# Kernel optimization log

Hardware: AMD Instinct MI355X
Metric: run time of the kernel (lower is better)

The kernel has to match this reference:

```python
import jax, jax.numpy as jnp
import numpy as np

EMBED_DIM = 1024
NUM_HEADS = 16
HEAD_DIM = EMBED_DIM // NUM_HEADS


def setup_inputs() -> dict:
    key = jax.random.key(0)
    ks = jax.random.split(key, 11)
    B, S, D = 2, 2048, EMBED_DIM
    s = 1.0 / np.sqrt(D)
    inp = {
        "query": jax.random.normal(ks[0], (B, S, D), jnp.float32),
        "key": jax.random.normal(ks[1], (B, S, D), jnp.float32),
        "value": jax.random.normal(ks[2], (B, S, D), jnp.float32),
        # torch Linear weights: [out, in]
        "Wq": jax.random.normal(ks[3], (D, D), jnp.float32) * s,
        "bq": jnp.zeros((D,), jnp.float32),
        "Wk": jax.random.normal(ks[4], (D, D), jnp.float32) * s,
        "bk": jnp.zeros((D,), jnp.float32),
        "Wv": jax.random.normal(ks[5], (D, D), jnp.float32) * s,
        "bv": jnp.zeros((D,), jnp.float32),
        "Wo": jax.random.normal(ks[6], (D, D), jnp.float32) * s,
        "bo": jnp.zeros((D,), jnp.float32),
    }
    return inp


def reference(query, key, value, Wq, bq, Wk, bk, Wv, bv, Wo, bo):
    B, Q, D = query.shape
    K = key.shape[1]
    H, Hd = NUM_HEADS, HEAD_DIM
    # NOTE: source divides by scaling = head_dim**-0.5, i.e. multiplies by sqrt(head_dim)
    scaling = float(Hd) ** (-0.5)

    q = (query @ Wq.T + bq).reshape(B, Q, H, Hd).transpose(0, 2, 1, 3)  # [B,H,Q,Hd]
    k = (key @ Wk.T + bk).reshape(B, K, H, Hd).transpose(0, 2, 1, 3)    # [B,H,K,Hd]
    v = (value @ Wv.T + bv).reshape(B, K, H, Hd).transpose(0, 2, 1, 3)  # [B,H,K,Hd]

    scores = jnp.einsum("bhqd,bhkd->bhqk", q, k) / scaling
    attn = jax.nn.softmax(scores, axis=-1)  # dropout=0 (eval)
    out = jnp.einsum("bhqk,bhkd->bhqd", attn, v)
    out = out.transpose(0, 2, 1, 3).reshape(B, Q, D)
    return out @ Wo.T + bo
```

## Files before the change

### kernel.cpp

```cpp
#include <hip/hip_runtime.h>
#include <type_traits>
#include <utility>

#define B_ 2
#define S_ 2048
#define D_ 1024
#define H_ 16
#define HD_ 64
#define KDIM 1024

typedef __attribute__((ext_vector_type(8))) short    s16x8;
typedef __attribute__((ext_vector_type(8))) _Float16 h16x8;
typedef __attribute__((ext_vector_type(4))) float    f32x4;
typedef __attribute__((ext_vector_type(16))) float   f32x16;
typedef __attribute__((ext_vector_type(4))) int      i32x4;
typedef __attribute__((ext_vector_type(2))) int      i32x2;

template <typename T, typename = void> struct mfma_takes : std::false_type {};
template <typename T>
struct mfma_takes<T, std::void_t<decltype(__builtin_amdgcn_mfma_f32_16x16x32_f16(
    std::declval<T>(), std::declval<T>(), std::declval<f32x4>(), 0, 0, 0))>>
    : std::true_type {};
using frag8 = std::conditional_t<mfma_takes<h16x8>::value, h16x8, s16x8>;

__device__ __forceinline__ f32x4 mfma_f16(frag8 a, frag8 b, f32x4 c) {
  return __builtin_amdgcn_mfma_f32_16x16x32_f16(a, b, c, 0, 0, 0);
}
__device__ __forceinline__ f32x16 mfma32(frag8 a, frag8 b, f32x16 c) {
  return __builtin_amdgcn_mfma_f32_32x32x16_f16(a, b, c, 0, 0, 0);
}

__device__ __forceinline__ short f2h(float f) {
  _Float16 h = (_Float16)f;
  short s; __builtin_memcpy(&s, &h, 2);
  return s;
}
__device__ __forceinline__ int pk2h(float a, float b) {
  auto p = __builtin_amdgcn_cvt_pkrtz(a, b);
  int r; __builtin_memcpy(&r, &p, 4); return r;
}
__device__ __forceinline__ frag8 ld_frag(const short* p) {
  return __builtin_bit_cast(frag8, *(const i32x4*)p);
}
__device__ __forceinline__ float fast_exp2(float x) {
  return __builtin_amdgcn_exp2f(x);
}
__device__ __forceinline__ void pl32swap(int& a, int& b) {
  asm volatile("v_permlane32_swap_b32 %0, %1" : "+v"(a), "+v"(b));
}

typedef __attribute__((address_space(1))) const void gvoid;
typedef __attribute__((address_space(3))) void lvoid;
__device__ __forceinline__ void async_copy16(const void* g, void* l) {
  __builtin_amdgcn_global_load_lds((gvoid*)g, (lvoid*)l, 16, 0, 0);
}

#define RAW_BARRIER() asm volatile("s_barrier" ::: "memory")
#define WAITCNT_VM(n) asm volatile("s_waitcnt vmcnt(" #n ")" ::: "memory")

__global__ __launch_bounds__(256)
void conv_w(const float* __restrict__ Wq, const float* __restrict__ Wk,
            const float* __restrict__ Wv, const float* __restrict__ Wo,
            short* __restrict__ wq, short* __restrict__ wk,
            short* __restrict__ wv, short* __restrict__ wo) {
  const int blk = blockIdx.x;
  const float* src; short* dst; int base;
  if (blk < 512)        { src = Wq; dst = wq; base = blk; }
  else if (blk < 1024)  { src = Wk; dst = wk; base = blk - 512; }
  else if (blk < 1536)  { src = Wv; dst = wv; base = blk - 1024; }
  else                  { src = Wo; dst = wo; base = blk - 1536; }
  const int i = base * 2048 + threadIdx.x * 8;
  float4 a0 = *(const float4*)(src + i);
  float4 a1 = *(const float4*)(src + i + 4);
  short h[8] = { f2h(a0.x), f2h(a0.y), f2h(a0.z), f2h(a0.w),
                 f2h(a1.x), f2h(a1.y), f2h(a1.z), f2h(a1.w) };
  i32x4 ph; __builtin_memcpy(&ph, h, 16);
  *(i32x4*)(dst + i) = ph;
}

__global__ __launch_bounds__(256, 3)
void gemm_qkv(const float* __restrict__ Aq, const float* __restrict__ Ak,
              const float* __restrict__ Av, const short* __restrict__ wq,
              const short* __restrict__ wk, const short* __restrict__ wv,
              const float* __restrict__ bq, const float* __restrict__ bk,
              const float* __restrict__ bv, short* __restrict__ Qf,
              short* __restrict__ Kf, short* __restrict__ Vt, float QS) {
  __shared__ short As[3 * 4096];
  __shared__ short Bs[3 * 4096];

  const int blk = blockIdx.x;
  const int xcd = blk & 7, i = blk >> 3;
  const int p = (i >> 3) * 8 + xcd;
  const int bn = i & 7;
  const int z = p >> 5, bm = p & 31;
  const float* Af = z == 0 ? Aq : z == 1 ? Ak : Av;
  const short* Wp = z == 0 ? wq : z == 1 ? wk : wv;
  const float* bias = z == 0 ? bq : z == 1 ? bk : bv;
  short* Out = z == 0 ? Qf : z == 1 ? Kf : Vt;
  const float scale = z == 0 ? QS : 1.0f;
  const int omode = z == 2 ? 2 : 1;

  const int t = threadIdx.x, wave = t >> 6, lane = t & 63;
  const int laneN = lane & 15, quad = lane >> 4;
  const int wm = wave & 1, wn = wave >> 1;

  f32x4 acc[4][4];
#pragma unroll
  for (int i2 = 0; i2 < 4; ++i2)
#pragma unroll
    for (int j = 0; j < 4; ++j)
#pragma unroll
      for (int r = 0; r < 4; ++r) acc[i2][j][r] = 0.f;

  const int ch0 = t, ch1 = 256 + t;
  const int ar0 = ch0 >> 2, ag0 = (ch0 & 3) ^ ((ar0 >> 1) & 3);
  const int ar1 = ch1 >> 2, ag1 = (ch1 & 3) ^ ((ar1 >> 1) & 3);
  const float* ap0 = Af + (size_t)(bm * 128 + ar0) * KDIM + ag0 * 8;
  const float* ap1 = Af + (size_t)(bm * 128 + ar1) * KDIM + ag1 * 8;

  f32x4 rA0a, rA0b, rA1a, rA1b;

  auto loadA = [&](int kk) {
    rA0a = *(const f32x4*)(ap0 + kk);
    rA0b = *(const f32x4*)(ap0 + kk + 4);
    rA1a = *(const f32x4*)(ap1 + kk);
    rA1b = *(const f32x4*)(ap1 + kk + 4);
  };
  auto writeA = [&](int slot) {
    short pk[8];
    pk[0] = f2h(rA0a[0]); pk[1] = f2h(rA0a[1]);
    pk[2] = f2h(rA0a[2]); pk[3] = f2h(rA0a[3]);
    pk[4] = f2h(rA0b[0]); pk[5] = f2h(rA0b[1]);
    pk[6] = f2h(rA0b[2]); pk[7] = f2h(rA0b[3]);
    i32x4 w0; __builtin_memcpy(&w0, pk, 16);
    *(i32x4*)(As + slot * 4096 + ch0 * 8) = w0;
    pk[0] = f2h(rA1a[0]); pk[1] = f2h(rA1a[1]);
    pk[2] = f2h(rA1a[2]); pk[3] = f2h(rA1a[3]);
    pk[4] = f2h(rA1b[0]); pk[5] = f2h(rA1b[1]);
    pk[6] = f2h(rA1b[2]); pk[7] = f2h(rA1b[3]);
    i32x4 w1; __builtin_memcpy(&w1, pk, 16);
    *(i32x4*)(As + slot * 4096 + ch1 * 8) = w1;
  };
  auto stageB = [&](int slot, int kk) {
#pragma unroll
    for (int j = 0; j < 2; ++j) {
      const int chunk = j * 256 + t;
      const int row = chunk >> 2;
      const int gg = (chunk & 3) ^ ((row >> 1) & 3);
      async_copy16(Wp + (size_t)(bn * 128 + row) * KDIM + kk + gg * 8,
                   Bs + slot * 4096 + chunk * 8);
    }
  };

  loadA(0);
  writeA(0);
  loadA(32);
  stageB(0, 0);
  stageB(1, 32);

  int buf = 0;
  for (int kk = 0; kk < KDIM; kk += 32) {
    if (kk + 64 < KDIM) {
      WAITCNT_VM(2);
      int ns = buf + 1; if (ns >= 3) ns -= 3;
      writeA(ns);
      loadA(kk + 64);
      int nb = buf + 2; if (nb >= 3) nb -= 3;
      stageB(nb, kk + 64);
    } else if (kk + 32 < KDIM) {
      WAITCNT_VM(2);
      int ns = buf + 1; if (ns >= 3) ns -= 3;
      writeA(ns);
    } else {
      WAITCNT_VM(0);
    }
    RAW_BARRIER();

    frag8 aF[4], bF[4];
#pragma unroll
    for (int mi = 0; mi < 4; ++mi) {
      const int row = wm * 64 + mi * 16 + laneN;
      aF[mi] = ld_frag(As + buf * 4096 + row * 32 +
                       ((quad ^ ((row >> 1) & 3)) * 8));
    }
#pragma unroll
    for (int ni = 0; ni < 4; ++ni) {
      const int row = wn * 64 + ni * 16 + laneN;
      bF[ni] = ld_frag(Bs + buf * 4096 + row * 32 +
                       ((quad ^ ((row >> 1) & 3)) * 8));
    }
#pragma unroll
    for (int mi = 0; mi < 4; ++mi)
#pragma unroll
      for (int ni = 0; ni < 4; ++ni)
        acc[mi][ni] = mfma_f16(aF[mi], bF[ni], acc[mi][ni]);
    RAW_BARRIER();
    buf = buf + 1 == 3 ? 0 : buf + 1;
  }

  short* scr = As + wave * 1152;
  const int h = bn * 2 + wn;
  if (omode == 2) {
    const int bidx = bm >> 4;
    const int sbase = (bm * 128 + wm * 64) & 2047;
#pragma unroll
    for (int ni = 0; ni < 4; ++ni) {
      const float bb = bias[bn * 128 + wn * 64 + ni * 16 + laneN];
#pragma unroll
      for (int mi = 0; mi < 4; ++mi) {
        short pk[4];
#pragma unroll
        for (int r = 0; r < 4; ++r) pk[r] = f2h(acc[mi][ni][r] + bb);
        i32x2 w; __builtin_memcpy(&w, pk, 8);
        *(i32x2*)(scr + laneN * 72 + mi * 16 + quad * 4) = w;
      }
#pragma unroll
      for (int j = 0; j < 2; ++j) {
        const int ff = lane * 2 + j, hdr = ff >> 3, ch = ff & 7;
        i32x4 v = *(const i32x4*)(scr + hdr * 72 + ch * 8);
        *(i32x4*)(Vt + (((size_t)(bidx * H_ + h)) * HD_ + ni * 16 + hdr) * S_ +
                  sbase + ch * 8) = v;
      }
    }
  } else {
#pragma unroll
    for (int mi = 0; mi < 4; ++mi) {
#pragma unroll
      for (int ni = 0; ni < 4; ++ni) {
        const float bb = bias[bn * 128 + wn * 64 + ni * 16 + laneN];
#pragma unroll
        for (int r = 0; r < 4; ++r)
          scr[(quad * 4 + r) * 72 + ni * 16 + laneN] =
              f2h((acc[mi][ni][r] + bb) * scale);
      }
#pragma unroll
      for (int j = 0; j < 2; ++j) {
        const int ff = lane * 2 + j, row = ff >> 3, ch = ff & 7;
        const int rowg = bm * 128 + wm * 64 + mi * 16 + row;
        const int bidx = rowg >> 11, s = rowg & 2047;
        i32x4 v = *(const i32x4*)(scr + row * 72 + ch * 8);
        *(i32x4*)(Out + (((size_t)(bidx * H_ + h)) * S_ + s) * HD_ + ch * 8) = v;
      }
    }
  }
}

__global__ __launch_bounds__(256, 3)
void gemm_out(const short* __restrict__ Ap, const short* __restrict__ Wp,
              const float* __restrict__ bias, float* __restrict__ Out) {
  __shared__ short As[2 * 8192];
  __shared__ short Bs[2 * 4096];
  const int blk = blockIdx.x;
  const int xcd = blk & 7, i = blk >> 3;
  const int bm = (i >> 4) * 8 + xcd;
  const int bn = i & 15;

  const int t = threadIdx.x, wave = t >> 6, lane = t & 63;
  const int laneN = lane & 15, quad = lane >> 4;
  const int wm = wave & 1, wn = wave >> 1;

  f32x4 acc[4][2];
#pragma unroll
  for (int i2 = 0; i2 < 4; ++i2)
#pragma unroll
    for (int j = 0; j < 2; ++j)
#pragma unroll
      for (int r = 0; r < 4; ++r) acc[i2][j][r] = 0.f;

  auto stage = [&](int buf, int kk) {
#pragma unroll
    for (int j = 0; j < 4; ++j) {
      const int c = j * 256 + t;
      const int row = c >> 3, g = (c & 7) ^ (row & 7);
      async_copy16(Ap + (size_t)(bm * 128 + row) * KDIM + kk + g * 8,
                   As + buf * 8192 + c * 8);
    }
#pragma unroll
    for (int j = 0; j < 2; ++j) {
      const int c = j * 256 + t;
      const int row = c >> 3, g = (c & 7) ^ (row & 7);
      async_copy16(Wp + (size_t)(bn * 64 + row) * KDIM + kk + g * 8,
                   Bs + buf * 4096 + c * 8);
    }
  };

  int offA[4][2], offB[2][2];
#pragma unroll
  for (int mi = 0; mi < 4; ++mi) {
    const int row = wm * 64 + mi * 16 + laneN;
#pragma unroll
    for (int ks = 0; ks < 2; ++ks)
      offA[mi][ks] = row * 64 + (((quad + 4 * ks) ^ (row & 7)) * 8);
  }
#pragma unroll
  for (int ni = 0; ni < 2; ++ni) {
    const int row = wn * 32 + ni * 16 + laneN;
#pragma unroll
    for (int ks = 0; ks < 2; ++ks)
      offB[ni][ks] = row * 64 + (((quad + 4 * ks) ^ (row & 7)) * 8);
  }

  stage(0, 0);
  int buf = 0;
  for (int kk = 0; kk < KDIM; kk += 64) {
    if (kk + 64 < KDIM) {
      stage(buf ^ 1, kk + 64);
      WAITCNT_VM(6);
    } else {
      WAITCNT_VM(0);
    }
    RAW_BARRIER();

    frag8 aF[4][2], bF[2][2];
#pragma unroll
    for (int mi = 0; mi < 4; ++mi) {
      aF[mi][0] = ld_frag(As + buf * 8192 + offA[mi][0]);
      aF[mi][1] = ld_frag(As + buf * 8192 + offA[mi][1]);
    }
#pragma unroll
    for (int ni = 0; ni < 2; ++ni) {
      bF[ni][0] = ld_frag(Bs + buf * 4096 + offB[ni][0]);
      bF[ni][1] = ld_frag(Bs + buf * 4096 + offB[ni][1]);
    }
#pragma unroll
    for (int mi = 0; mi < 4; ++mi)
#pragma unroll
      for (int ni = 0; ni < 2; ++ni) {
        acc[mi][ni] = mfma_f16(aF[mi][0], bF[ni][0], acc[mi][ni]);
        acc[mi][ni] = mfma_f16(aF[mi][1], bF[ni][1], acc[mi][ni]);
      }
    RAW_BARRIER();
    buf ^= 1;
  }

  float* scr = (float*)As + wave * 576;
#pragma unroll
  for (int mi = 0; mi < 4; ++mi) {
#pragma unroll
    for (int ni = 0; ni < 2; ++ni) {
      const float bb = bias[bn * 64 + wn * 32 + ni * 16 + laneN];
#pragma unroll
      for (int r = 0; r < 4; ++r)
        scr[(quad * 4 + r) * 36 + ni * 16 + laneN] = acc[mi][ni][r] + bb;
    }
#pragma unroll
    for (int j = 0; j < 2; ++j) {
      const int ff = lane * 2 + j, row = ff >> 3, ch = ff & 7;
      const int rowg = bm * 128 + wm * 64 + mi * 16 + row;
      f32x4 v = *(const f32x4*)(scr + row * 36 + ch * 4);
      *(f32x4*)(Out + (size_t)rowg * 1024 + bn * 64 + wn * 32 + ch * 4) = v;
    }
  }
}

__global__ __launch_bounds__(256, 2)
void attn(const short* __restrict__ Qf, const short* __restrict__ Kf,
          const short* __restrict__ Vt_, short* __restrict__ Ow) {
  __shared__ short Ks[4 * 4096];
  __shared__ short Vts[4 * 4096];

  const int blk = blockIdx.x;
  const int xcd = blk & 7, local = blk >> 3;
  const int pair = xcd * 4 + (local >> 4);
  const int h = pair & 15, b = pair >> 4, qt = local & 15;
  const size_t head = ((size_t)b * H_ + h) * (size_t)S_ * HD_;

  const int t = threadIdx.x;
  const int wave = t >> 6, lane = t & 63;
  const int l31 = lane & 31, hi = lane >> 5;

  const int q0 = qt * 128 + wave * 32;

  frag8 qf[4];
  {
    const short* qp = Qf + head + (size_t)(q0 + l31) * HD_ + hi * 8;
#pragma unroll
    for (int ds = 0; ds < 4; ++ds) qf[ds] = ld_frag(qp + ds * 16);
  }

  f32x16 o0, o1;
#pragma unroll
  for (int r = 0; r < 16; ++r) { o0[r] = 0.f; o1[r] = 0.f; }
  float m_r = -1e30f, l_r = 0.f;

  const int c0 = t, c1 = 256 + t;
  const int r0 = c0 >> 3, gg0 = (c0 & 7) ^ (r0 & 7);
  const int r1 = c1 >> 3, gg1 = (c1 & 7) ^ (r1 & 7);
  const short* kp0 = Kf + head + (size_t)r0 * HD_ + gg0 * 8;
  const short* kp1 = Kf + head + (size_t)r1 * HD_ + gg1 * 8;
  const short* vp0 = Vt_ + head + (size_t)r0 * S_ + gg0 * 8;
  const short* vp1 = Vt_ + head + (size_t)r1 * S_ + gg1 * 8;
  const int d0 = c0 * 8, d1 = c1 * 8;

  int off2[2][4];
#pragma unroll
  for (int hf = 0; hf < 2; ++hf) {
    const int row = hf * 32 + l31;
#pragma unroll
    for (int j = 0; j < 4; ++j)
      off2[hf][j] = row * 64 + (((j * 2 + hi) ^ (row & 7)) * 8);
  }

  async_copy16(kp0, Ks + d0);  async_copy16(kp1, Ks + d1);
  async_copy16(vp0, Vts + d0); async_copy16(vp1, Vts + d1);
  kp0 += 4096; kp1 += 4096; vp0 += 64; vp1 += 64;
  async_copy16(kp0, Ks + 4096 + d0);  async_copy16(kp1, Ks + 4096 + d1);
  async_copy16(vp0, Vts + 4096 + d0); async_copy16(vp1, Vts + 4096 + d1);
  kp0 += 4096; kp1 += 4096; vp0 += 64; vp1 += 64;

#define ATTN_TILE(B0, STG)                                                   \
  {                                                                          \
    if (STG == 1) {                                                          \
      const int nb = ((B0) + 2) & 3;                                         \
      async_copy16(kp0, Ks + nb * 4096 + d0);                                \
      async_copy16(kp1, Ks + nb * 4096 + d1);                                \
      async_copy16(vp0, Vts + nb * 4096 + d0);                               \
      async_copy16(vp1, Vts + nb * 4096 + d1);                               \
      kp0 += 4096; kp1 += 4096; vp0 += 64; vp1 += 64;                        \
      WAITCNT_VM(8);                                                         \
    } else if (STG == 2) {                                                   \
      WAITCNT_VM(4);                                                         \
    } else {                                                                 \
      WAITCNT_VM(0);                                                         \
    }                                                                        \
    RAW_BARRIER();                                                           \
    const short* KbS = Ks + (B0) * 4096;                                     \
    const short* VbS = Vts + (B0) * 4096;                                    \
                  \
    f32x16 sA, sB;                                                           \
    _Pragma("unroll")                                                        \
    for (int r = 0; r < 16; ++r) { sA[r] = 0.f; sB[r] = 0.f; }               \
    __builtin_amdgcn_s_setprio(1);                                           \
    _Pragma("unroll")                                                        \
    for (int ds = 0; ds < 4; ++ds) {                                         \
      frag8 ka = ld_frag(KbS + off2[0][ds]);                                 \
      frag8 kb = ld_frag(KbS + off2[1][ds]);                                 \
      sA = mfma32(ka, qf[ds], sA);                                           \
      sB = mfma32(kb, qf[ds], sB);                                           \
    }                                                                        \
    __builtin_amdgcn_s_setprio(0);                                           \
                 \
    {                                                                        \
      float mA = sA[0], mB = sB[0];                                          \
      _Pragma("unroll")                                                      \
      for (int r = 1; r < 16; ++r) {                                         \
        mA = fmaxf(mA, sA[r]); mB = fmaxf(mB, sB[r]);                        \
      }                                                                      \
      float mx = fmaxf(mA, mB);                                              \
      mx = fmaxf(mx, __shfl_xor(mx, 32));                                    \
      if (__any(mx > m_r + 8.f)) {                                           \
        const float mn = fmaxf(m_r, mx);                                     \
        const float al = fast_exp2(m_r - mn);                                \
        m_r = mn; l_r *= al;                                                 \
        _Pragma("unroll")                                                    \
        for (int r = 0; r < 16; ++r) { o0[r] *= al; o1[r] *= al; }           \
      }                                                                      \
      float rs = 0.f;                                                        \
      _Pragma("unroll")                                                      \
      for (int r = 0; r < 16; ++r) {                                         \
        const float pa = fast_exp2(sA[r] - m_r);                             \
        const float pb = fast_exp2(sB[r] - m_r);                             \
        sA[r] = pa; sB[r] = pb; rs += pa + pb;                               \
      }                                                                      \
      rs += __shfl_xor(rs, 32);                                              \
      l_r += rs;                                                             \
    }                                                                        \
       \
    frag8 pf0, pf1, pf2, pf3;                                                \
    {                                                                        \
      int w0, w1, w2, w3; i32x4 fw;                                          \
      w0 = pk2h(sA[0], sA[1]);   w1 = pk2h(sA[2], sA[3]);                    \
      w2 = pk2h(sA[4], sA[5]);   w3 = pk2h(sA[6], sA[7]);                    \
      pl32swap(w0, w2); pl32swap(w1, w3);                                    \
      fw[0] = w0; fw[1] = w1; fw[2] = w2; fw[3] = w3;                        \
      pf0 = __builtin_bit_cast(frag8, fw);                                   \
      w0 = pk2h(sA[8], sA[9]);   w1 = pk2h(sA[10], sA[11]);                  \
      w2 = pk2h(sA[12], sA[13]); w3 = pk2h(sA[14], sA[15]);                  \
      pl32swap(w0, w2); pl32swap(w1, w3);                                    \
      fw[0] = w0; fw[1] = w1; fw[2] = w2; fw[3] = w3;                        \
      pf1 = __builtin_bit_cast(frag8, fw);                                   \
      w0 = pk2h(sB[0], sB[1]);   w1 = pk2h(sB[2], sB[3]);                    \
      w2 = pk2h(sB[4], sB[5]);   w3 = pk2h(sB[6], sB[7]);                    \
      pl32swap(w0, w2); pl32swap(w1, w3);                                    \
      fw[0] = w0; fw[1] = w1; fw[2] = w2; fw[3] = w3;                        \
      pf2 = __builtin_bit_cast(frag8, fw);                                   \
      w0 = pk2h(sB[8], sB[9]);   w1 = pk2h(sB[10], sB[11]);                  \
      w2 = pk2h(sB[12], sB[13]); w3 = pk2h(sB[14], sB[15]);                  \
      pl32swap(w0, w2); pl32swap(w1, w3);                                    \
      fw[0] = w0; fw[1] = w1; fw[2] = w2; fw[3] = w3;                        \
      pf3 = __builtin_bit_cast(frag8, fw);                                   \
    }                                                                        \
                        \
    __builtin_amdgcn_s_setprio(1);                                           \
    {                                                                        \
      frag8 va, vb;                                                          \
      va = ld_frag(VbS + off2[0][0]); o0 = mfma32(va, pf0, o0);              \
      vb = ld_frag(VbS + off2[1][0]); o1 = mfma32(vb, pf0, o1);              \
      va = ld_frag(VbS + off2[0][1]); o0 = mfma32(va, pf1, o0);              \
      vb = ld_frag(VbS + off2[1][1]); o1 = mfma32(vb, pf1, o1);              \
      va = ld_frag(VbS + off2[0][2]); o0 = mfma32(va, pf2, o0);              \
      vb = ld_frag(VbS + off2[1][2]); o1 = mfma32(vb, pf2, o1);              \
      va = ld_frag(VbS + off2[0][3]); o0 = mfma32(va, pf3, o0);              \
      vb = ld_frag(VbS + off2[1][3]); o1 = mfma32(vb, pf3, o1);              \
    }                                                                        \
    __builtin_amdgcn_s_setprio(0);                                           \
  }

  for (int it = 0; it < 7; ++it) {
    ATTN_TILE(0, 1)
    ATTN_TILE(1, 1)
    ATTN_TILE(2, 1)
    ATTN_TILE(3, 1)
  }
  ATTN_TILE(0, 1)
  ATTN_TILE(1, 1)
  ATTN_TILE(2, 2)
  ATTN_TILE(3, 0)
#undef ATTN_TILE

  {
    const float inv = 1.0f / l_r;
    short* dst = Ow + ((size_t)b * S_ + q0 + l31) * D_ + h * HD_ + hi * 4;
#pragma unroll
    for (int rg = 0; rg < 4; ++rg) {
      i32x2 w;
      w[0] = pk2h(o0[rg * 4 + 0] * inv, o0[rg * 4 + 1] * inv);
      w[1] = pk2h(o0[rg * 4 + 2] * inv, o0[rg * 4 + 3] * inv);
      *(i32x2*)(dst + rg * 8) = w;
      i32x2 w2;
      w2[0] = pk2h(o1[rg * 4 + 0] * inv, o1[rg * 4 + 1] * inv);
      w2[1] = pk2h(o1[rg * 4 + 2] * inv, o1[rg * 4 + 3] * inv);
      *(i32x2*)(dst + 32 + rg * 8) = w2;
    }
  }
}

extern "C" void kernel_launch(void* const* d_in, const int* in_sizes, int n_in,
                              void* d_out, int out_size, void* d_ws, size_t ws_size,
                              hipStream_t stream) {
  const float* q  = (const float*)d_in[0];
  const float* k  = (const float*)d_in[1];
  const float* v  = (const float*)d_in[2];
  const float* Wq = (const float*)d_in[3];
  const float* bq = (const float*)d_in[4];
  const float* Wk = (const float*)d_in[5];
  const float* bk = (const float*)d_in[6];
  const float* Wv = (const float*)d_in[7];
  const float* bv = (const float*)d_in[8];
  const float* Wo = (const float*)d_in[9];
  const float* bo = (const float*)d_in[10];

  const size_t NTOK = (size_t)B_ * S_ * D_;
  const size_t NW   = (size_t)D_ * D_;
  short* p = (short*)d_ws;
  short* wq = p; p += NW;    short* wk = p; p += NW;
  short* wv = p; p += NW;    short* wo = p; p += NW;
  short* Qf = p; p += NTOK;  short* Kf = p; p += NTOK;
  short* Vt = p; p += NTOK;  short* Ow = p; p += NTOK;

  dim3 blk(256);

  conv_w<<<2048, blk, 0, stream>>>(Wq, Wk, Wv, Wo, wq, wk, wv, wo);

  const float QS = 11.541560327111707f;
  gemm_qkv<<<768, blk, 0, stream>>>(q, k, v, wq, wk, wv, bq, bk, bv,
                                    Qf, Kf, Vt, QS);

  attn<<<512, dim3(256), 0, stream>>>(Qf, Kf, Vt, Ow);

  gemm_out<<<512, blk, 0, stream>>>(Ow, wo, bo, (float*)d_out);
}
```

Before: 233.9 us.

## Deepen A-operand register prefetch to two stages in QKV projection GEMM

The fp32 A-tile global loads in the QKV projection GEMM are now double-buffered in registers, so each load is issued two k-steps ahead instead of one. The main loop is unrolled by two with explicit register sets, plus a peeled prologue and epilogue with adjusted vmcnt waits. This aims to hide more global-load latency behind the MFMA work. The cost is more VGPRs for the extra register stage, which could lower occupancy.

```diff
diff --git a/kernel.cpp b/kernel.cpp
--- a/kernel.cpp
+++ b/kernel.cpp
@@ -47,6 +47,12 @@
 }
 __device__ __forceinline__ void pl32swap(int& a, int& b) {
   asm volatile("v_permlane32_swap_b32 %0, %1" : "+v"(a), "+v"(b));
+}
+__device__ __forceinline__ void cvt_store8(f32x4 va, f32x4 vb, short* dst) {
+  short pk[8] = { f2h(va[0]), f2h(va[1]), f2h(va[2]), f2h(va[3]),
+                  f2h(vb[0]), f2h(vb[1]), f2h(vb[2]), f2h(vb[3]) };
+  i32x4 w; __builtin_memcpy(&w, pk, 16);
+  *(i32x4*)dst = w;
 }
 
 typedef __attribute__((address_space(1))) const void gvoid;
@@ -118,29 +124,36 @@
   const float* ap0 = Af + (size_t)(bm * 128 + ar0) * KDIM + ag0 * 8;
   const float* ap1 = Af + (size_t)(bm * 128 + ar1) * KDIM + ag1 * 8;
 
-  f32x4 rA0a, rA0b, rA1a, rA1b;
-
-  auto loadA = [&](int kk) {
-    rA0a = *(const f32x4*)(ap0 + kk);
-    rA0b = *(const f32x4*)(ap0 + kk + 4);
-    rA1a = *(const f32x4*)(ap1 + kk);
-    rA1b = *(const f32x4*)(ap1 + kk + 4);
-  };
-  auto writeA = [&](int slot) {
-    short pk[8];
-    pk[0] = f2h(rA0a[0]); pk[1] = f2h(rA0a[1]);
-    pk[2] = f2h(rA0a[2]); pk[3] = f2h(rA0a[3]);
-    pk[4] = f2h(rA0b[0]); pk[5] = f2h(rA0b[1]);
-    pk[6] = f2h(rA0b[2]); pk[7] = f2h(rA0b[3]);
-    i32x4 w0; __builtin_memcpy(&w0, pk, 16);
-    *(i32x4*)(As + slot * 4096 + ch0 * 8) = w0;
-    pk[0] = f2h(rA1a[0]); pk[1] = f2h(rA1a[1]);
-    pk[2] = f2h(rA1a[2]); pk[3] = f2h(rA1a[3]);
-    pk[4] = f2h(rA1b[0]); pk[5] = f2h(rA1b[1]);
-    pk[6] = f2h(rA1b[2]); pk[7] = f2h(rA1b[3]);
-    i32x4 w1; __builtin_memcpy(&w1, pk, 16);
-    *(i32x4*)(As + slot * 4096 + ch1 * 8) = w1;
-  };
+  f32x4 s0_0, s0_1, s0_2, s0_3;
+  f32x4 s1_0, s1_1, s1_2, s1_3;
+
+#define LOADA(S, KK)                                                         \
+  do {                                                                       \
+    if (S) {                                                                 \
+      s1_0 = *(const f32x4*)(ap0 + (KK));                                    \
+      s1_1 = *(const f32x4*)(ap0 + (KK) + 4);                                \
+      s1_2 = *(const f32x4*)(ap1 + (KK));                                    \
+      s1_3 = *(const f32x4*)(ap1 + (KK) + 4);                                \
+    } else {                                                                 \
+      s0_0 = *(const f32x4*)(ap0 + (KK));                                    \
+      s0_1 = *(const f32x4*)(ap0 + (KK) + 4);                                \
+      s0_2 = *(const f32x4*)(ap1 + (KK));                                    \
+      s0_3 = *(const f32x4*)(ap1 + (KK) + 4);                                \
+    }                                                                        \
+  } while (0)
+
+#define WRITEA(S, SLOT)                                                      \
+  do {                                                                       \
+    short* dA = As + (SLOT) * 4096;                                          \
+    if (S) {                                                                 \
+      cvt_store8(s1_0, s1_1, dA + ch0 * 8);                                  \
+      cvt_store8(s1_2, s1_3, dA + ch1 * 8);                                  \
+    } else {                                                                 \
+      cvt_store8(s0_0, s0_1, dA + ch0 * 8);                                  \
+      cvt_store8(s0_2, s0_3, dA + ch1 * 8);                                  \
+    }                                                                        \
+  } while (0)
+
   auto stageB = [&](int slot, int kk) {
 #pragma unroll
     for (int j = 0; j < 2; ++j) {
@@ -152,51 +165,86 @@
     }
   };
 
-  loadA(0);
-  writeA(0);
-  loadA(32);
+  auto compute = [&](int cb) {
+    frag8 aF[4], bF[4];
+#pragma unroll
+    for (int mi = 0; mi < 4; ++mi) {
+      const int row = wm * 64 + mi * 16 + laneN;
+      aF[mi] = ld_frag(As + cb * 4096 + row * 32 +
+                       ((quad ^ ((row >> 1) & 3)) * 8));
+    }
+#pragma unroll
+    for (int ni = 0; ni < 4; ++ni) {
+      const int row = wn * 64 + ni * 16 + laneN;
+      bF[ni] = ld_frag(Bs + cb * 4096 + row * 32 +
+                       ((quad ^ ((row >> 1) & 3)) * 8));
+    }
+#pragma unroll
+    for (int mi = 0; mi < 4; ++mi)
+#pragma unroll
+      for (int ni = 0; ni < 4; ++ni)
+        acc[mi][ni] = mfma_f16(aF[mi], bF[ni], acc[mi][ni]);
+  };
+
+  LOADA(0, 0);
+  LOADA(1, 32);
   stageB(0, 0);
   stageB(1, 32);
-
-  int buf = 0;
-  for (int kk = 0; kk < KDIM; kk += 32) {
-    if (kk + 64 < KDIM) {
-      WAITCNT_VM(2);
-      int ns = buf + 1; if (ns >= 3) ns -= 3;
-      writeA(ns);
-      loadA(kk + 64);
-      int nb = buf + 2; if (nb >= 3) nb -= 3;
-      stageB(nb, kk + 64);
-    } else if (kk + 32 < KDIM) {
-      WAITCNT_VM(2);
-      int ns = buf + 1; if (ns >= 3) ns -= 3;
-      writeA(ns);
-    } else {
-      WAITCNT_VM(0);
-    }
-    RAW_BARRIER();
-
-    frag8 aF[4], bF[4];
-#pragma unroll
-    for (int mi = 0; mi < 4; ++mi) {
-      const int row = wm * 64 + mi * 16 + laneN;
-      aF[mi] = ld_frag(As + buf * 4096 + row * 32 +
-                       ((quad ^ ((row >> 1) & 3)) * 8));
-    }
-#pragma unroll
-    for (int ni = 0; ni < 4; ++ni) {
-      const int row = wn * 64 + ni * 16 + laneN;
-      bF[ni] = ld_frag(Bs + buf * 4096 + row * 32 +
-                       ((quad ^ ((row >> 1) & 3)) * 8));
-    }
-#pragma unroll
-    for (int mi = 0; mi < 4; ++mi)
-#pragma unroll
-      for (int ni = 0; ni < 4; ++ni)
-        acc[mi][ni] = mfma_f16(aF[mi], bF[ni], acc[mi][ni]);
-    RAW_BARRIER();
-    buf = buf + 1 == 3 ? 0 : buf + 1;
-  }
+  WAITCNT_VM(8);
+  WRITEA(0, 0);
+  LOADA(0, 64);
+
+  int buf = 0, kk = 0;
+
+#define QKV_ITER(S)                                                          \
+  {                                                                          \
+    WAITCNT_VM(6);                               \
+    int ns = buf + 1; if (ns >= 3) ns -= 3;                                  \
+    WRITEA(S, ns);                                                           \
+    LOADA(S, kk + 96);                                                       \
+    int nb = ns + 1; if (nb >= 3) nb -= 3;                                   \
+    stageB(nb, kk + 64);                                                     \
+    RAW_BARRIER();                                                           \
+    compute(buf);                                                            \
+    RAW_BARRIER();                                                           \
+    buf = ns; kk += 32;                                                      \
+  }
+
+  for (int it = 0; it < 14; ++it) {
+    QKV_ITER(1)
+    QKV_ITER(0)
+  }
+  QKV_ITER(1)
+#undef QKV_ITER
+
+  {
+    WAITCNT_VM(6);
+    int ns = buf + 1; if (ns >= 3) ns -= 3;
+    WRITEA(0, ns);
+    int nb = ns + 1; if (nb >= 3) nb -= 3;
+    stageB(nb, 992);
+    RAW_BARRIER();
+    compute(buf);
+    RAW_BARRIER();
+    buf = ns;
+  }
+  {
+    WAITCNT_VM(2);
+    int ns = buf + 1; if (ns >= 3) ns -= 3;
+    WRITEA(1, ns);
+    RAW_BARRIER();
+    compute(buf);
+    RAW_BARRIER();
+    buf = ns;
+  }
+  {
+    WAITCNT_VM(0);
+    RAW_BARRIER();
+    compute(buf);
+    RAW_BARRIER();
+  }
+#undef LOADA
+#undef WRITEA
 
   short* scr = As + wave * 1152;
   const int h = bn * 2 + wn;
```

Result: faster. 220.0 us (-5.9%).
